# Optimization experiments

Measured on AMD Instinct MI355X. Metric: run time of the kernel, lower is better.

## Reference

```python
import jax, jax.numpy as jnp
import numpy as np

Q, C, D = 4096, 4096, 1024
EPS = 1e-6  # torch.nn.PairwiseDistance default eps, added to (x1 - x2)


def _cdist_l2(a, b):
    # ||(a + EPS) - b||_2 for all pairs, via GEMM formulation.
    a = a + EPS
    sq = (jnp.sum(a * a, axis=1)[:, None]
          + jnp.sum(b * b, axis=1)[None, :]
          - 2.0 * a @ b.T)
    return jnp.sqrt(jnp.maximum(sq, 0.0))


def setup_inputs() -> dict:
    key = jax.random.key(0)
    k1, k2, k3, k4, k5, k6 = jax.random.split(key, 6)
    return {
        "context_rgb_features": jax.random.normal(k1, (C, D), dtype=jnp.float32),
        "context_flow_features": jax.random.normal(k2, (C, D), dtype=jnp.float32),
        "target_rgb_features": jax.random.normal(k3, (Q, D), dtype=jnp.float32),
        "target_flow_features": jax.random.normal(k4, (Q, D), dtype=jnp.float32),
        "c_r": jax.random.uniform(k5, (Q,), dtype=jnp.float32, minval=0.1, maxval=1.0),
        "c_f": jax.random.uniform(k6, (Q,), dtype=jnp.float32, minval=0.1, maxval=1.0),
    }


def reference(context_rgb_features, context_flow_features,
              target_rgb_features, target_flow_features, c_r, c_f):
    denom = c_r + c_f
    w_r = (c_r / denom)[:, None]   # [Q, 1]
    w_f = (c_f / denom)[:, None]
    d_rgb = _cdist_l2(target_rgb_features, context_rgb_features)    # [Q, C]
    d_flow = _cdist_l2(target_flow_features, context_flow_features)  # [Q, C]
    posterior = w_r * jnp.exp(-d_rgb) + w_f * jnp.exp(-d_flow)
    return posterior / jnp.sum(posterior, axis=1, keepdims=True)
```

## Files before the change

### kernel.cpp

```cpp
#include <hip/hip_runtime.h>
#include <hip/hip_bf16.h>

#define QN 4096
#define CN 4096
#define DN 1024
#define EPSV 1e-6f

#define BM 128
#define BN 128
#define BK 64
#define TILE (BM * BK)

#define MATSZ ((size_t)QN * DN)
#define SFP 132

using bf16x8 = __attribute__((ext_vector_type(8))) __bf16;
using f32x4  = __attribute__((ext_vector_type(4))) float;

static __device__ __forceinline__ unsigned short f2bf_rne(float x) {
  unsigned int u = __float_as_uint(x);
  unsigned int r = (u + 0x7FFFu + ((u >> 16) & 1u)) >> 16;
  return (unsigned short)r;
}
static __device__ __forceinline__ float bf2f(unsigned short h) {
  return __uint_as_float(((unsigned int)h) << 16);
}

static __device__ __forceinline__ void gload_lds16(const unsigned short* g, unsigned short* l) {
  __builtin_amdgcn_global_load_lds(
      (const __attribute__((address_space(1))) unsigned int*)g,
      (__attribute__((address_space(3))) unsigned int*)l, 16, 0, 0);
}


__global__ void prep_kernel(const float* __restrict__ tgt_r, const float* __restrict__ tgt_f,
                            const float* __restrict__ ctx_r, const float* __restrict__ ctx_f,
                            unsigned short* __restrict__ ws16, float* __restrict__ norms) {
  const int t = threadIdx.x;
  const int w = t >> 6;
  const int lane = t & 63;
  const int row = blockIdx.x * 4 + w;
  const int mat = blockIdx.y;
  const float* src; float eps;
  switch (mat) {
    case 0:  src = tgt_r; eps = EPSV; break;
    case 1:  src = tgt_f; eps = EPSV; break;
    case 2:  src = ctx_r; eps = 0.f;  break;
    default: src = ctx_f; eps = 0.f;  break;
  }
  unsigned short* hi = ws16 + (size_t)mat * MATSZ;
  float* nrm = norms + (size_t)mat * QN;
  const size_t base = (size_t)row * DN;
  const float4* s4 = (const float4*)(src + base);
  ushort4* d4 = (ushort4*)(hi + base);
  float ss = 0.f;
#pragma unroll
  for (int i = 0; i < 4; ++i) {
    float4 v = s4[lane + 64 * i];
    float a[4] = {v.x + eps, v.y + eps, v.z + eps, v.w + eps};
    unsigned short hh[4];
#pragma unroll
    for (int k = 0; k < 4; ++k) {
      hh[k] = f2bf_rne(a[k]);
      float f = bf2f(hh[k]);
      ss += f * f;
    }
    d4[lane + 64 * i] = make_ushort4(hh[0], hh[1], hh[2], hh[3]);
  }
#pragma unroll
  for (int o = 32; o > 0; o >>= 1) ss += __shfl_down(ss, o);
  if (lane == 0) nrm[row] = ss;
}

__global__ __launch_bounds__(256, 2)
void gemm_kernel(const unsigned short* __restrict__ ws16,
                 const float* __restrict__ norms,
                 const float* __restrict__ c_r, const float* __restrict__ c_f,
                 float* __restrict__ out) {
  __shared__ unsigned short S[4 * TILE];

  const int t = threadIdx.x;
  const int lane = t & 63;
  const int wid = t >> 6;
  const int wr = wid >> 1;
  const int wc = wid & 1;
  const int row0 = blockIdx.y * BM;
  const int col0 = blockIdx.x * BN;

  f32x4 acc[2][4][4];
#pragma unroll
  for (int m = 0; m < 2; ++m)
#pragma unroll
    for (int i = 0; i < 4; ++i)
#pragma unroll
      for (int j = 0; j < 4; ++j)
        acc[m][i][j] = (f32x4){0.f, 0.f, 0.f, 0.f};

  const int srw = lane >> 3;
  const int sch = (lane & 7) ^ srw;
  const size_t src_off = (size_t)(wid * 8 + srw) * DN + sch * 8;
  const size_t aoff = (size_t)row0 * DN + src_off;
  const size_t boff = (size_t)col0 * DN + src_off;
  unsigned short* ldsW = S + wid * 8 * BK;

  const unsigned short* pAr = ws16 + 0 * MATSZ + aoff;
  const unsigned short* pAf = ws16 + 1 * MATSZ + aoff;
  const unsigned short* pBr = ws16 + 2 * MATSZ + boff;
  const unsigned short* pBf = ws16 + 3 * MATSZ + boff;

  const int lr = lane & 15;
  const int lq = lane >> 4;
  const int sc0 = (lq ^ (lr & 7)) * 8;
  int ra[4], rb[4];
#pragma unroll
  for (int i = 0; i < 4; ++i) {
    ra[i] = (wr * 64 + i * 16 + lr) * BK + sc0;
    rb[i] = (wc * 64 + i * 16 + lr) * BK + sc0;
  }
#define KS1(x) ((x) ^ 32)

  for (int kc = 0; kc < DN / BK; ++kc) {
    const int k = kc * BK;
    __syncthreads();
#pragma unroll
    for (int it = 0; it < 4; ++it) {
      const size_t g = (size_t)it * 32 * DN + k;
      unsigned short* l = ldsW + it * 32 * BK;
      gload_lds16(pAr + g, l + 0 * TILE);
      gload_lds16(pAf + g, l + 1 * TILE);
      gload_lds16(pBr + g, l + 2 * TILE);
      gload_lds16(pBf + g, l + 3 * TILE);
    }
    __syncthreads();

#pragma unroll
    for (int ksub = 0; ksub < 2; ++ksub) {
      bf16x8 ar[4], af[4], br[4], bf[4];
#pragma unroll
      for (int i = 0; i < 4; ++i) {
        const int oa = ksub ? KS1(ra[i]) : ra[i];
        const int ob = ksub ? KS1(rb[i]) : rb[i];
        ar[i] = *(const bf16x8*)(S + 0 * TILE + oa);
        af[i] = *(const bf16x8*)(S + 1 * TILE + oa);
        br[i] = *(const bf16x8*)(S + 2 * TILE + ob);
        bf[i] = *(const bf16x8*)(S + 3 * TILE + ob);
      }
#pragma unroll
      for (int i = 0; i < 4; ++i)
#pragma unroll
        for (int j = 0; j < 4; ++j) {
          acc[0][i][j] = __builtin_amdgcn_mfma_f32_16x16x32_bf16(ar[i], br[j], acc[0][i][j], 0, 0, 0);
          acc[1][i][j] = __builtin_amdgcn_mfma_f32_16x16x32_bf16(af[i], bf[j], acc[1][i][j], 0, 0, 0);
        }
    }
  }

  const float* tn_r = norms;
  const float* tn_f = norms + QN;
  const float* cn_r = norms + 2 * QN;
  const float* cn_f = norms + 3 * QN;

  float cnr[4], cnf[4];
#pragma unroll
  for (int j = 0; j < 4; ++j) {
    const int cc = col0 + wc * 64 + j * 16 + lr;
    cnr[j] = cn_r[cc];
    cnf[j] = cn_f[cc];
  }

  float* Sf = (float*)S;
  const int lrow = t >> 3;
  const int c0 = (t & 7) * 16;
  const int grow_base = row0 + (lrow >> 4) * 64 + (lrow & 15);

  __syncthreads();

#pragma unroll
  for (int i = 0; i < 4; ++i) {
    if (i > 0) __syncthreads();
#pragma unroll
    for (int r = 0; r < 4; ++r) {
      const int tq = row0 + wr * 64 + i * 16 + lq * 4 + r;
      const float tnr = tn_r[tq];
      const float tnf = tn_f[tq];
      const float cr = c_r[tq], cf = c_f[tq];
      const float inv = 1.f / (cr + cf);
      const float wgr = cr * inv, wgf = cf * inv;
      float* sfrow = Sf + (wr * 16 + lq * 4 + r) * SFP + wc * 64 + lr;
#pragma unroll
      for (int j = 0; j < 4; ++j) {
        const float sr_ = tnr + cnr[j] - 2.f * acc[0][i][j][r];
        const float sf_ = tnf + cnf[j] - 2.f * acc[1][i][j][r];
        const float dr = sqrtf(fmaxf(sr_, 0.f));
        const float df = sqrtf(fmaxf(sf_, 0.f));
        sfrow[j * 16] = wgr * __expf(-dr) + wgf * __expf(-df);
      }
    }
    __syncthreads();
    const float* src = Sf + lrow * SFP + c0;
    float4 v0 = ((const float4*)src)[0];
    float4 v1 = ((const float4*)src)[1];
    float4 v2 = ((const float4*)src)[2];
    float4 v3 = ((const float4*)src)[3];
    float4* dst = (float4*)(out + (size_t)(grow_base + i * 16) * CN + col0 + c0);
    dst[0] = v0; dst[1] = v1; dst[2] = v2; dst[3] = v3;
  }
}

__global__ void norm_kernel(float* __restrict__ out) {
  const int t = threadIdx.x;
  const int w = t >> 6;
  const int lane = t & 63;
  const int row = blockIdx.x * 4 + w;
  float4* p = (float4*)(out + (size_t)row * CN);
  float4 v[16];
  float s = 0.f;
#pragma unroll
  for (int i = 0; i < 16; ++i) {
    v[i] = p[lane + 64 * i];
    s += v[i].x + v[i].y + v[i].z + v[i].w;
  }
#pragma unroll
  for (int o = 32; o > 0; o >>= 1) s += __shfl_down(s, o);
  const float inv = 1.f / __shfl(s, 0);
#pragma unroll
  for (int i = 0; i < 16; ++i) {
    v[i].x *= inv; v[i].y *= inv; v[i].z *= inv; v[i].w *= inv;
    p[lane + 64 * i] = v[i];
  }
}

extern "C" void kernel_launch(void* const* d_in, const int* in_sizes, int n_in,
                              void* d_out, int out_size, void* d_ws, size_t ws_size,
                              hipStream_t stream) {
  const float* ctx_r = (const float*)d_in[0];
  const float* ctx_f = (const float*)d_in[1];
  const float* tgt_r = (const float*)d_in[2];
  const float* tgt_f = (const float*)d_in[3];
  const float* c_r   = (const float*)d_in[4];
  const float* c_f   = (const float*)d_in[5];
  float* out = (float*)d_out;
  unsigned short* ws16 = (unsigned short*)d_ws;
  float* norms = (float*)(ws16 + 4 * MATSZ);

  prep_kernel<<<dim3(QN / 4, 4), 256, 0, stream>>>(tgt_r, tgt_f, ctx_r, ctx_f, ws16, norms);
  gemm_kernel<<<dim3(CN / BN, QN / BM), 256, 0, stream>>>(ws16, norms, c_r, c_f, out);
  norm_kernel<<<QN / 4, 256, 0, stream>>>(out);
}
```

Measured before the change: 236.0 us.

## Write GEMM epilogue directly to global and use one block per row in prep/norm

The GEMM epilogue no longer stages results through LDS for coalesced float4 stores. Each lane now writes scalar values straight to global memory, and the context norms are read inline instead of being preloaded. The prep and norm kernels switch from one wave per row to one 256-thread block per row, with a shared-memory reduction. This removes the LDS round trip and its barriers, but the output writes become strided scalar stores, which may hurt write coalescing for the large output.

Result: faster. 218.7 us (-7.3%).

```diff
diff --git a/kernel.cpp b/kernel.cpp
--- a/kernel.cpp
+++ b/kernel.cpp
@@ -12,7 +12,6 @@
 #define TILE (BM * BK)
 
 #define MATSZ ((size_t)QN * DN)
-#define SFP 132
 
 using bf16x8 = __attribute__((ext_vector_type(8))) __bf16;
 using f32x4  = __attribute__((ext_vector_type(4))) float;
@@ -36,11 +35,9 @@
 __global__ void prep_kernel(const float* __restrict__ tgt_r, const float* __restrict__ tgt_f,
                             const float* __restrict__ ctx_r, const float* __restrict__ ctx_f,
                             unsigned short* __restrict__ ws16, float* __restrict__ norms) {
+  const int row = blockIdx.x;
+  const int mat = blockIdx.y;
   const int t = threadIdx.x;
-  const int w = t >> 6;
-  const int lane = t & 63;
-  const int row = blockIdx.x * 4 + w;
-  const int mat = blockIdx.y;
   const float* src; float eps;
   switch (mat) {
     case 0:  src = tgt_r; eps = EPSV; break;
@@ -51,25 +48,24 @@
   unsigned short* hi = ws16 + (size_t)mat * MATSZ;
   float* nrm = norms + (size_t)mat * QN;
   const size_t base = (size_t)row * DN;
-  const float4* s4 = (const float4*)(src + base);
-  ushort4* d4 = (ushort4*)(hi + base);
+  float4 v = ((const float4*)(src + base))[t];
+  float a[4] = {v.x + eps, v.y + eps, v.z + eps, v.w + eps};
   float ss = 0.f;
-#pragma unroll
-  for (int i = 0; i < 4; ++i) {
-    float4 v = s4[lane + 64 * i];
-    float a[4] = {v.x + eps, v.y + eps, v.z + eps, v.w + eps};
-    unsigned short hh[4];
-#pragma unroll
-    for (int k = 0; k < 4; ++k) {
-      hh[k] = f2bf_rne(a[k]);
-      float f = bf2f(hh[k]);
-      ss += f * f;
-    }
-    d4[lane + 64 * i] = make_ushort4(hh[0], hh[1], hh[2], hh[3]);
-  }
+  unsigned short hh[4];
+#pragma unroll
+  for (int k = 0; k < 4; ++k) {
+    hh[k] = f2bf_rne(a[k]);
+    float f = bf2f(hh[k]);
+    ss += f * f;
+  }
+  ((ushort4*)(hi + base))[t] = make_ushort4(hh[0], hh[1], hh[2], hh[3]);
+
 #pragma unroll
   for (int o = 32; o > 0; o >>= 1) ss += __shfl_down(ss, o);
-  if (lane == 0) nrm[row] = ss;
+  __shared__ float red[4];
+  if ((t & 63) == 0) red[t >> 6] = ss;
+  __syncthreads();
+  if (t == 0) nrm[row] = red[0] + red[1] + red[2] + red[3];
 }
 
 __global__ __launch_bounds__(256, 2)
@@ -160,24 +156,8 @@
   const float* cn_r = norms + 2 * QN;
   const float* cn_f = norms + 3 * QN;
 
-  float cnr[4], cnf[4];
-#pragma unroll
-  for (int j = 0; j < 4; ++j) {
-    const int cc = col0 + wc * 64 + j * 16 + lr;
-    cnr[j] = cn_r[cc];
-    cnf[j] = cn_f[cc];
-  }
-
-  float* Sf = (float*)S;
-  const int lrow = t >> 3;
-  const int c0 = (t & 7) * 16;
-  const int grow_base = row0 + (lrow >> 4) * 64 + (lrow & 15);
-
-  __syncthreads();
-
-#pragma unroll
-  for (int i = 0; i < 4; ++i) {
-    if (i > 0) __syncthreads();
+#pragma unroll
+  for (int i = 0; i < 4; ++i) {
 #pragma unroll
     for (int r = 0; r < 4; ++r) {
       const int tq = row0 + wr * 64 + i * 16 + lq * 4 + r;
@@ -186,47 +166,41 @@
       const float cr = c_r[tq], cf = c_f[tq];
       const float inv = 1.f / (cr + cf);
       const float wgr = cr * inv, wgf = cf * inv;
-      float* sfrow = Sf + (wr * 16 + lq * 4 + r) * SFP + wc * 64 + lr;
 #pragma unroll
       for (int j = 0; j < 4; ++j) {
-        const float sr_ = tnr + cnr[j] - 2.f * acc[0][i][j][r];
-        const float sf_ = tnf + cnf[j] - 2.f * acc[1][i][j][r];
+        const int cc = col0 + wc * 64 + j * 16 + lr;
+        const float sr_ = tnr + cn_r[cc] - 2.f * acc[0][i][j][r];
+        const float sf_ = tnf + cn_f[cc] - 2.f * acc[1][i][j][r];
         const float dr = sqrtf(fmaxf(sr_, 0.f));
         const float df = sqrtf(fmaxf(sf_, 0.f));
-        sfrow[j * 16] = wgr * __expf(-dr) + wgf * __expf(-df);
+        const float p = wgr * __expf(-dr) + wgf * __expf(-df);
+        out[(size_t)tq * CN + cc] = p;
       }
     }
-    __syncthreads();
-    const float* src = Sf + lrow * SFP + c0;
-    float4 v0 = ((const float4*)src)[0];
-    float4 v1 = ((const float4*)src)[1];
-    float4 v2 = ((const float4*)src)[2];
-    float4 v3 = ((const float4*)src)[3];
-    float4* dst = (float4*)(out + (size_t)(grow_base + i * 16) * CN + col0 + c0);
-    dst[0] = v0; dst[1] = v1; dst[2] = v2; dst[3] = v3;
   }
 }
 
 __global__ void norm_kernel(float* __restrict__ out) {
+  const int row = blockIdx.x;
   const int t = threadIdx.x;
-  const int w = t >> 6;
-  const int lane = t & 63;
-  const int row = blockIdx.x * 4 + w;
   float4* p = (float4*)(out + (size_t)row * CN);
-  float4 v[16];
+  float4 v[4];
   float s = 0.f;
 #pragma unroll
-  for (int i = 0; i < 16; ++i) {
-    v[i] = p[lane + 64 * i];
+  for (int i = 0; i < 4; ++i) {
+    v[i] = p[t + 256 * i];
     s += v[i].x + v[i].y + v[i].z + v[i].w;
   }
 #pragma unroll
   for (int o = 32; o > 0; o >>= 1) s += __shfl_down(s, o);
-  const float inv = 1.f / __shfl(s, 0);
-#pragma unroll
-  for (int i = 0; i < 16; ++i) {
+  __shared__ float red[4];
+  if ((t & 63) == 0) red[t >> 6] = s;
+  __syncthreads();
+  const float inv = 1.f / (red[0] + red[1] + red[2] + red[3]);
+#pragma unroll
+  for (int i = 0; i < 4; ++i) {
     v[i].x *= inv; v[i].y *= inv; v[i].z *= inv; v[i].w *= inv;
-    p[lane + 64 * i] = v[i];
+    p[t + 256 * i] = v[i];
   }
 }
 
@@ -243,7 +217,7 @@
   unsigned short* ws16 = (unsigned short*)d_ws;
   float* norms = (float*)(ws16 + 4 * MATSZ);
 
-  prep_kernel<<<dim3(QN / 4, 4), 256, 0, stream>>>(tgt_r, tgt_f, ctx_r, ctx_f, ws16, norms);
+  prep_kernel<<<dim3(QN, 4), 256, 0, stream>>>(tgt_r, tgt_f, ctx_r, ctx_f, ws16, norms);
   gemm_kernel<<<dim3(CN / BN, QN / BM), 256, 0, stream>>>(ws16, norms, c_r, c_f, out);
-  norm_kernel<<<QN / 4, 256, 0, stream>>>(out);
-}
+  norm_kernel<<<QN, 256, 0, stream>>>(out);
+}
```
